# Kernel optimization log

Hardware: AMD Instinct MI355X
Metric: run time of the kernel (lower is better)

The kernel has to match this reference:

```python
import jax, jax.numpy as jnp
import numpy as np

B, S, E = 8, 2048, 768
N, H = 12, 64
INIT = 0.02
IGNORE = -100000.0


def setup_inputs() -> dict:
    key = jax.random.key(0)
    ks = jax.random.split(key, 5)
    return {
        "normalized_resid_pre": jax.random.normal(ks[0], (B, S, E), jnp.float32),
        "W_Q": jax.random.normal(ks[1], (N, E, H), jnp.float32) * INIT,
        "W_K": jax.random.normal(ks[2], (N, E, H), jnp.float32) * INIT,
        "W_V": jax.random.normal(ks[3], (N, E, H), jnp.float32) * INIT,
        "W_O": jax.random.normal(ks[4], (N, H, E), jnp.float32) * INIT,
        "b_Q": jnp.zeros((N, H), jnp.float32),
        "b_K": jnp.zeros((N, H), jnp.float32),
        "b_V": jnp.zeros((N, H), jnp.float32),
        "b_O": jnp.zeros((E,), jnp.float32),
    }


def reference(normalized_resid_pre, W_Q, W_K, W_V, W_O, b_Q, b_K, b_V, b_O):
    x = normalized_resid_pre
    b, s, e = x.shape
    d_head = W_Q.shape[-1]
    q = jnp.einsum('bse,neh->bsnh', x, W_Q) + b_Q  # [b, sq, n, h]
    k = jnp.einsum('bse,neh->bsnh', x, W_K) + b_K
    v = jnp.einsum('bse,neh->bsnh', x, W_V) + b_V
    scores = jnp.einsum('bqnh,bknh->bnqk', q, k) / jnp.sqrt(jnp.float32(d_head))
    mask = jnp.tril(jnp.ones((s, s), jnp.float32))  # [sq, sk]
    masked = mask * scores + (1.0 - mask) * IGNORE
    probs = jax.nn.softmax(masked, axis=-1)
    z = jnp.einsum('bnqk,bknh->bqnh', probs, v)
    # sum over heads of per-head output projection + bias
    out = jnp.einsum('bqnh,nhe->bqe', z, W_O) + b_O
    return out
```

## Files before the change

kernel.cpp:

```cpp
#include <hip/hip_runtime.h>
#include <hip/hip_bf16.h>
#include <stdint.h>


#define B_ 8
#define S_ 2048
#define E_ 768
#define NHEADS 12
#define HD 64
#define BS (B_*S_)
#define NHD (NHEADS*HD)

typedef short bf16x8 __attribute__((ext_vector_type(8)));
typedef short bf16x4 __attribute__((ext_vector_type(4)));
typedef float f32x4  __attribute__((ext_vector_type(4)));
typedef __hip_bfloat16 bf16;

typedef const __attribute__((address_space(1))) char* as1_t;
typedef __attribute__((address_space(3))) char* as3_t;

__device__ __forceinline__ f32x4 mfma16(bf16x8 a, bf16x8 b, f32x4 c) {
    return __builtin_amdgcn_mfma_f32_16x16x32_bf16(a, b, c, 0, 0, 0);
}
__device__ __forceinline__ bf16x8 ld8(const bf16* p) {
    return *reinterpret_cast<const bf16x8*>(p);
}
__device__ __forceinline__ void gload16(const bf16* g, bf16* l) {
    __builtin_amdgcn_global_load_lds((as1_t)g, (as3_t)l, 16, 0, 0);
}
__device__ __forceinline__ bf16x8 pack8(f32x4 a, f32x4 b) {
    union { bf16x8 v; __hip_bfloat162 h[4]; } u;
    u.h[0] = __float22bfloat162_rn(make_float2(a[0], a[1]));
    u.h[1] = __float22bfloat162_rn(make_float2(a[2], a[3]));
    u.h[2] = __float22bfloat162_rn(make_float2(b[0], b[1]));
    u.h[3] = __float22bfloat162_rn(make_float2(b[2], b[3]));
    return u.v;
}

__global__ __launch_bounds__(256) void prep_kernel(
    const float* __restrict__ x,  const float* __restrict__ Wq,
    const float* __restrict__ Wk, const float* __restrict__ Wv,
    const float* __restrict__ Wo,
    bf16* __restrict__ xb,  bf16* __restrict__ WqT, bf16* __restrict__ WkT,
    bf16* __restrict__ WvT, bf16* __restrict__ WoT)
{
    const int tid = blockIdx.x * 256 + threadIdx.x;
    const int nth = gridDim.x * 256;
    for (int i = tid; i < BS*E_; i += nth)
        xb[i] = __float2bfloat16(x[i]);
    for (int i = tid; i < NHD*E_; i += nth) {
        const int c = i / E_;
        const int e = i - c*E_;
        const int n = c >> 6, h = c & 63;
        const int src = (n*E_ + e)*HD + h;
        WqT[i] = __float2bfloat16(Wq[src]);
        WkT[i] = __float2bfloat16(Wk[src]);
        WvT[i] = __float2bfloat16(Wv[src]);
        WoT[e*NHD + c] = __float2bfloat16(Wo[i]);
    }
}


#define FENCE() asm volatile("" ::: "memory")
#define LGKM0() do { asm volatile("s_waitcnt lgkmcnt(0)" ::: "memory"); \
                     __builtin_amdgcn_sched_barrier(0); } while (0)
#define VMCNT0() asm volatile("s_waitcnt vmcnt(0)" ::: "memory")
#define MIN11(x) ((x) < 11 ? (x) : 11)

#define A_ELEM(kh, rg) (((kh)*8 + (rg))*512)
#define B_ELEM(kh, rg) (((kh)*12 + (rg))*512)

#define STG_A(dst, gbase, kt) do {                                                \
    const bf16* _s = (gbase) + (size_t)(w*16 + l16)*768 + (kt)*64 + quad*8;       \
    gload16(_s,      &(dst)[A_ELEM(0, w)]);                                       \
    gload16(_s + 32, &(dst)[A_ELEM(1, w)]);                                       \
} while (0)

#define STG_B(dst, gbase, kt) do {                                                \
    const bf16* _s = (gbase) + (size_t)(l16)*768 + (kt)*64 + quad*8;              \
    const int _k1 = (w < 4) ? 0 : 1;                                              \
    const int _r1 = (w < 4) ? (w + 8) : (w - 4);                                  \
    gload16(_s + (size_t)(w*16)*768,        &(dst)[B_ELEM(0, w)]);                \
    gload16(_s + (size_t)(_r1*16)*768 + _k1*32, &(dst)[B_ELEM(_k1, _r1)]);        \
    gload16(_s + (size_t)((w+4)*16)*768 + 32,   &(dst)[B_ELEM(1, w+4)]);          \
} while (0)

#define KTILE(bufA, bufB, nA, nB, ktn, Ab, Bb) do {                               \
                                          \
    _Pragma("unroll") for (int n = 0; n < 3; ++n)                                 \
    _Pragma("unroll") for (int ks = 0; ks < 2; ++ks)                              \
        bfr[n][ks] = ld8(&(bufB)[((ks)*12 + wn*3 + n)*512 + lane*8]);             \
    {                                                                             \
        bf16x8 afr[2][2];                                                         \
        _Pragma("unroll") for (int m = 0; m < 2; ++m)                             \
        _Pragma("unroll") for (int ks = 0; ks < 2; ++ks)                          \
            afr[m][ks] = ld8(&(bufA)[((ks)*8 + wm*4 + m)*512 + lane*8]);          \
        STG_A(nA, Ab, ktn);                                                       \
        LGKM0();                                                                  \
        __builtin_amdgcn_s_setprio(1);                                            \
        _Pragma("unroll") for (int m = 0; m < 2; ++m)                             \
        _Pragma("unroll") for (int n = 0; n < 3; ++n)                             \
        _Pragma("unroll") for (int ks = 0; ks < 2; ++ks)                          \
            acc[m][n] = mfma16(afr[m][ks], bfr[n][ks], acc[m][n]);                \
        __builtin_amdgcn_s_setprio(0);                                            \
    }                                                                             \
                                                    \
    {                                                                             \
        bf16x8 afr[2][2];                                                         \
        _Pragma("unroll") for (int m = 0; m < 2; ++m)                             \
        _Pragma("unroll") for (int ks = 0; ks < 2; ++ks)                          \
            afr[m][ks] = ld8(&(bufA)[((ks)*8 + wm*4 + 2 + m)*512 + lane*8]);      \
        STG_B(nB, Bb, ktn);                                                       \
        LGKM0();                                                                  \
        __builtin_amdgcn_s_setprio(1);                                            \
        _Pragma("unroll") for (int m = 0; m < 2; ++m)                             \
        _Pragma("unroll") for (int n = 0; n < 3; ++n)                             \
        _Pragma("unroll") for (int ks = 0; ks < 2; ++ks)                          \
            acc[2+m][n] = mfma16(afr[m][ks], bfr[n][ks], acc[2+m][n]);            \
        __builtin_amdgcn_s_setprio(0);                                            \
    }                                                                             \
    VMCNT0();                                                                     \
    FENCE(); __builtin_amdgcn_s_barrier(); FENCE();                               \
} while (0)

#define GEMM128_BODY(Ab, Bb)                                                      \
    f32x4 acc[4][3];                                                              \
    _Pragma("unroll") for (int mf = 0; mf < 4; ++mf)                              \
    _Pragma("unroll") for (int nf = 0; nf < 3; ++nf)                              \
        acc[mf][nf] = (f32x4){0.f, 0.f, 0.f, 0.f};                                \
    bf16x8 bfr[3][2];                                                             \
    STG_A(sA0, Ab, 0); STG_B(sB0, Bb, 0);                                         \
    VMCNT0();                                                                     \
    FENCE(); __builtin_amdgcn_s_barrier(); FENCE();                               \
    _Pragma("unroll 1")                                                           \
    for (int i2 = 0; i2 < 6; ++i2) {                                              \
        const int kt0 = 2*i2;                                                     \
        KTILE(sA0, sB0, sA1, sB1, kt0 + 1,        Ab, Bb);                        \
        KTILE(sA1, sB1, sA0, sB0, MIN11(kt0 + 2), Ab, Bb);                        \
    }

__global__ __launch_bounds__(512, 4) void qkv_gemm256(
    const bf16* __restrict__ xb, const bf16* __restrict__ WT,
    const float* __restrict__ bq, const float* __restrict__ bk, const float* __restrict__ bv,
    bf16* __restrict__ Qb, bf16* __restrict__ Kb, bf16* __restrict__ VTb)
{
    __shared__ __align__(16) bf16 sA0[8192];
    __shared__ __align__(16) bf16 sA1[8192];
    __shared__ __align__(16) bf16 sB0[12288];
    __shared__ __align__(16) bf16 sB1[12288];

    const int tm = blockIdx.x, tn = blockIdx.y;
    const int lane = threadIdx.x & 63;
    const int w    = threadIdx.x >> 6;
    const int wm = w >> 2, wn = w & 3;
    const int l16 = lane & 15, quad = lane >> 4;
    const bf16* Ab = xb + (size_t)tm*128*E_;
    const bf16* Bb = WT + (size_t)tn*192*E_;

    GEMM128_BODY(Ab, Bb);

    const int mat = tn >> 2;
    const int cloc0 = (tn & 3)*192 + wn*48;
    const float* bias = (mat==0) ? bq : (mat==1) ? bk : bv;
    const float scale = (mat==0) ? 0.125f * 1.44269504088896340736f : 1.0f;
    bf16* dstQK = (mat==0) ? Qb : Kb;
    #pragma unroll
    for (int nf = 0; nf < 3; ++nf) {
        const int col = cloc0 + nf*16 + l16;
        const int hn = col >> 6, h = col & 63;
        const float bb = bias[col];
        #pragma unroll
        for (int mf = 0; mf < 4; ++mf) {
            const int row = tm*128 + wm*64 + mf*16 + quad*4;
            const int bi = row >> 11;
            const int s  = row & (S_-1);
            if (mat < 2) {
                bf16* d = dstQK + ((size_t)(bi*NHEADS + hn)*S_ + s)*HD + h;
                #pragma unroll
                for (int r = 0; r < 4; ++r)
                    d[(size_t)r*HD] = __float2bfloat16((acc[mf][nf][r] + bb)*scale);
            } else {
                bf16* d = VTb + ((size_t)(bi*NHEADS + hn)*HD + h)*S_ + s;
                union { bf16x4 v; bf16 e[4]; } u;
                #pragma unroll
                for (int r = 0; r < 4; ++r) u.e[r] = __float2bfloat16(acc[mf][nf][r] + bb);
                *reinterpret_cast<bf16x4*>(d) = u.v;
            }
        }
    }
}

__global__ __launch_bounds__(512, 4) void out_gemm256(
    const bf16* __restrict__ Z, const bf16* __restrict__ WoT,
    const float* __restrict__ bo, float* __restrict__ out)
{
    __shared__ __align__(16) bf16 sA0[8192];
    __shared__ __align__(16) bf16 sA1[8192];
    __shared__ __align__(16) bf16 sB0[12288];
    __shared__ __align__(16) bf16 sB1[12288];

    const int tm = blockIdx.x, tn = blockIdx.y;
    const int lane = threadIdx.x & 63;
    const int w    = threadIdx.x >> 6;
    const int wm = w >> 2, wn = w & 3;
    const int l16 = lane & 15, quad = lane >> 4;
    const bf16* Ab = Z   + (size_t)tm*128*NHD;
    const bf16* Bb = WoT + (size_t)tn*192*NHD;

    GEMM128_BODY(Ab, Bb);

    #pragma unroll
    for (int nf = 0; nf < 3; ++nf) {
        const int col = tn*192 + wn*48 + nf*16 + l16;
        const float bb = bo[col];
        #pragma unroll
        for (int mf = 0; mf < 4; ++mf) {
            const int row = tm*128 + wm*64 + mf*16 + quad*4;
            float* d = out + (size_t)row*E_ + col;
            #pragma unroll
            for (int r = 0; r < 4; ++r)
                d[(size_t)r*E_] = acc[mf][nf][r] + bb;
        }
    }
}

__global__ __launch_bounds__(256, 3) void attn_kernel(
    const bf16* __restrict__ Qb, const bf16* __restrict__ Kb,
    const bf16* __restrict__ VTb, bf16* __restrict__ Z)
{
    __shared__ __align__(16) bf16 sK[2][64*64];
    __shared__ __align__(16) bf16 sV[2][64*64];

    const int id = blockIdx.x;
    const int bx = id / 96;
    const int g  = id - bx*96;
    const int hn = g % NHEADS, b = g / NHEADS;
    const int tid  = threadIdx.x;
    const int w    = tid >> 6;
    const int lane = tid & 63;
    const int l16 = lane & 15, quad = lane >> 4;
    const size_t bn = (size_t)b*NHEADS + hn;

    const bf16* Qbase = Qb  + bn*S_*HD;
    const bf16* Kbase = Kb  + bn*S_*HD;
    const bf16* Vbase = VTb + bn*HD*S_;

    const int mA = tid, mB = tid + 256;
    const int rA = mA >> 3, cgA = mA & 7;
    const int rB = mB >> 3, cgB = mB & 7;
    const int slA = (rA*8 + ((cgA + rA + (rA>>3)) & 7)) * 8;
    const int slB = (rB*8 + ((cgB + rB + (rB>>3)) & 7)) * 8;
    const size_t vofA = (size_t)rA*S_ + cgA*8;
    const size_t vofB = (size_t)rB*S_ + cgB*8;

    const int kperm = (l16 >> 2)*8 + (l16 & 3);
    int kidx[2][2][2];
    #pragma unroll
    for (int c=0;c<2;c++)
        #pragma unroll
        for (int bg=0;bg<2;bg++)
            #pragma unroll
            for (int hf=0;hf<2;hf++) {
                const int r = 32*c + 4*bg + kperm;
                const int q = hf*4 + quad;
                kidx[c][bg][hf] = (r*8 + ((q + r + (r>>3)) & 7)) * 8;
            }
    int vidx[4][2];
    #pragma unroll
    for (int ht=0;ht<4;ht++)
        #pragma unroll
        for (int c=0;c<2;c++) {
            const int rho = ht*16 + l16;
            const int q = c*4 + quad;
            vidx[ht][c] = (rho*8 + ((q + rho + (rho>>3)) & 7)) * 8;
        }

    #pragma unroll
    for (int half = 0; half < 2; ++half) {
        const int qblk = half ? (S_/128 - 1 - bx) : bx;
        const int ktb  = 2*qblk + 1;
        const int ktw  = 2*qblk + (w >> 1);
        const int qbase = qblk*128 + w*32;

        bf16x8 bqf[2][2];
        #pragma unroll
        for (int qi=0;qi<2;qi++)
            #pragma unroll
            for (int hf=0;hf<2;hf++)
                bqf[qi][hf] = ld8(Qbase + (size_t)(qbase + qi*16 + l16)*HD + hf*32 + quad*8);

        f32x4 acc[2][4];
        #pragma unroll
        for (int qi=0;qi<2;qi++)
            #pragma unroll
            for (int ht=0;ht<4;ht++) acc[qi][ht] = (f32x4){0.f,0.f,0.f,0.f};
        float lsum[2] = {0.f, 0.f};

        bf16x8 k0 = ld8(Kbase + (size_t)mA*8);
        bf16x8 k1 = ld8(Kbase + (size_t)mB*8);
        bf16x8 v0 = ld8(Vbase + vofA);
        bf16x8 v1 = ld8(Vbase + vofB);
        *reinterpret_cast<bf16x8*>(&sK[0][slA]) = k0;
        *reinterpret_cast<bf16x8*>(&sK[0][slB]) = k1;
        *reinterpret_cast<bf16x8*>(&sV[0][slA]) = v0;
        *reinterpret_cast<bf16x8*>(&sV[0][slB]) = v1;
        __syncthreads();

        for (int kt = 0; kt <= ktb; ++kt) {
            if (kt < ktb) {
                const size_t kt1 = (size_t)(kt+1)*64;
                k0 = ld8(Kbase + kt1*HD + (size_t)mA*8);
                k1 = ld8(Kbase + kt1*HD + (size_t)mB*8);
                v0 = ld8(Vbase + vofA + kt1);
                v1 = ld8(Vbase + vofB + kt1);
            }
            if (kt <= ktw) {
                const bf16* kb = sK[kt & 1];
                const bf16* vb = sV[kt & 1];
                #pragma unroll
                for (int c=0;c<2;c++) {
                    const bf16x8 akA0 = ld8(kb + kidx[c][0][0]);
                    const bf16x8 akA1 = ld8(kb + kidx[c][0][1]);
                    const bf16x8 akB0 = ld8(kb + kidx[c][1][0]);
                    const bf16x8 akB1 = ld8(kb + kidx[c][1][1]);
                    bf16x8 av[4];
                    #pragma unroll
                    for (int ht=0;ht<4;ht++) av[ht] = ld8(vb + vidx[ht][c]);

                    #pragma unroll
                    for (int qi=0;qi<2;qi++) {
                        f32x4 s0 = (f32x4){0.f,0.f,0.f,0.f};
                        s0 = mfma16(akA0, bqf[qi][0], s0);
                        s0 = mfma16(akA1, bqf[qi][1], s0);
                        f32x4 s1 = (f32x4){0.f,0.f,0.f,0.f};
                        s1 = mfma16(akB0, bqf[qi][0], s1);
                        s1 = mfma16(akB1, bqf[qi][1], s1);
                        if (kt == ktw) {
                            const int q  = qbase + qi*16 + l16;
                            const int kb0 = kt*64 + c*32 + quad*8;
                            #pragma unroll
                            for (int r=0;r<4;r++) {
                                s0[r] = (kb0 + r     > q) ? -1e30f : s0[r];
                                s1[r] = (kb0 + 4 + r > q) ? -1e30f : s1[r];
                            }
                        }
                        float ls = 0.f;
                        #pragma unroll
                        for (int r=0;r<4;r++) {
                            s0[r] = __builtin_amdgcn_exp2f(s0[r]);
                            s1[r] = __builtin_amdgcn_exp2f(s1[r]);
                            ls += s0[r] + s1[r];
                        }
                        lsum[qi] += ls;
                        const bf16x8 pf = pack8(s0, s1);
                        #pragma unroll
                        for (int ht=0;ht<4;ht++)
                            acc[qi][ht] = mfma16(av[ht], pf, acc[qi][ht]);
                    }
                }
            }
            if (kt < ktb) {
                const int nb = (kt+1) & 1;
                *reinterpret_cast<bf16x8*>(&sK[nb][slA]) = k0;
                *reinterpret_cast<bf16x8*>(&sK[nb][slB]) = k1;
                *reinterpret_cast<bf16x8*>(&sV[nb][slA]) = v0;
                *reinterpret_cast<bf16x8*>(&sV[nb][slB]) = v1;
            }
            __syncthreads();
        }

        #pragma unroll
        for (int qi=0;qi<2;qi++) {
            float rs = lsum[qi];
            rs += __shfl_xor(rs, 16, 64);
            rs += __shfl_xor(rs, 32, 64);
            const float inv_l = 1.0f / rs;
            const int q = qbase + qi*16 + l16;
            bf16* zp = Z + ((size_t)b*S_ + q)*NHD + (size_t)hn*HD + quad*4;
            #pragma unroll
            for (int ht=0;ht<4;ht++) {
                union { bf16x4 v; bf16 e[4]; } u;
                #pragma unroll
                for (int r=0;r<4;r++) u.e[r] = __float2bfloat16(acc[qi][ht][r] * inv_l);
                *reinterpret_cast<bf16x4*>(zp + ht*16) = u.v;
            }
        }
    }
}

extern "C" void kernel_launch(void* const* d_in, const int* in_sizes, int n_in,
                              void* d_out, int out_size, void* d_ws, size_t ws_size,
                              hipStream_t stream)
{
    const float* x  = (const float*)d_in[0];
    const float* Wq = (const float*)d_in[1];
    const float* Wk = (const float*)d_in[2];
    const float* Wv = (const float*)d_in[3];
    const float* Wo = (const float*)d_in[4];
    const float* bq = (const float*)d_in[5];
    const float* bk = (const float*)d_in[6];
    const float* bv = (const float*)d_in[7];
    const float* bo = (const float*)d_in[8];
    float* out = (float*)d_out;

    char* ws = (char*)d_ws;
    size_t off = 0;
    auto alloc = [&](size_t bytes){ char* p = ws + off; off += (bytes + 255) & ~(size_t)255; return p; };
    bf16* xb  = (bf16*)alloc((size_t)BS*E_*2);
    bf16* WT  = (bf16*)alloc((size_t)3*NHD*E_*2);
    bf16* WoT = (bf16*)alloc((size_t)E_*NHD*2);
    bf16* Qb  = (bf16*)alloc((size_t)BS*NHD*2);
    bf16* Kb  = (bf16*)alloc((size_t)BS*NHD*2);
    bf16* VTb = (bf16*)alloc((size_t)BS*NHD*2);
    bf16* Zb  = (bf16*)alloc((size_t)BS*NHD*2);

    bf16* WqT = WT;
    bf16* WkT = WT + (size_t)NHD*E_;
    bf16* WvT = WT + (size_t)2*NHD*E_;

    prep_kernel<<<4096, 256, 0, stream>>>(x, Wq, Wk, Wv, Wo, xb, WqT, WkT, WvT, WoT);
    qkv_gemm256<<<dim3(BS/128, 12), 512, 0, stream>>>(xb, WT, bq, bk, bv, Qb, Kb, VTb);
    attn_kernel<<<768, 256, 0, stream>>>(Qb, Kb, VTb, Zb);
    out_gemm256<<<dim3(BS/128, E_/192), 512, 0, stream>>>(Zb, WoT, bo, out);
}
```

Measured before the change: 242.5 us.

## Replace LDS-staged GEMMs with direct global-to-register MFMA loads

Both projection GEMMs drop the double-buffered global_load_lds staging through shared memory. Each wave now loads its A and B fragments straight from global memory into registers for every k-tile. Tiles shrink to 128x96 with 4 waves per block, which doubles the grid. This removes LDS traffic and barriers, but each wave reloads operands with no sharing through shared memory, so it depends on cache hits and adds global-memory latency.

```diff
diff --git a/kernel.cpp b/kernel.cpp
--- a/kernel.cpp
+++ b/kernel.cpp
@@ -16,17 +16,11 @@
 typedef float f32x4  __attribute__((ext_vector_type(4)));
 typedef __hip_bfloat16 bf16;
 
-typedef const __attribute__((address_space(1))) char* as1_t;
-typedef __attribute__((address_space(3))) char* as3_t;
-
 __device__ __forceinline__ f32x4 mfma16(bf16x8 a, bf16x8 b, f32x4 c) {
     return __builtin_amdgcn_mfma_f32_16x16x32_bf16(a, b, c, 0, 0, 0);
 }
 __device__ __forceinline__ bf16x8 ld8(const bf16* p) {
     return *reinterpret_cast<const bf16x8*>(p);
-}
-__device__ __forceinline__ void gload16(const bf16* g, bf16* l) {
-    __builtin_amdgcn_global_load_lds((as1_t)g, (as3_t)l, 16, 0, 0);
 }
 __device__ __forceinline__ bf16x8 pack8(f32x4 a, f32x4 b) {
     union { bf16x8 v; __hip_bfloat162 h[4]; } u;
@@ -61,106 +55,43 @@
 }
 
 
-#define FENCE() asm volatile("" ::: "memory")
-#define LGKM0() do { asm volatile("s_waitcnt lgkmcnt(0)" ::: "memory"); \
-                     __builtin_amdgcn_sched_barrier(0); } while (0)
-#define VMCNT0() asm volatile("s_waitcnt vmcnt(0)" ::: "memory")
-#define MIN11(x) ((x) < 11 ? (x) : 11)
-
-#define A_ELEM(kh, rg) (((kh)*8 + (rg))*512)
-#define B_ELEM(kh, rg) (((kh)*12 + (rg))*512)
-
-#define STG_A(dst, gbase, kt) do {                                                \
-    const bf16* _s = (gbase) + (size_t)(w*16 + l16)*768 + (kt)*64 + quad*8;       \
-    gload16(_s,      &(dst)[A_ELEM(0, w)]);                                       \
-    gload16(_s + 32, &(dst)[A_ELEM(1, w)]);                                       \
-} while (0)
-
-#define STG_B(dst, gbase, kt) do {                                                \
-    const bf16* _s = (gbase) + (size_t)(l16)*768 + (kt)*64 + quad*8;              \
-    const int _k1 = (w < 4) ? 0 : 1;                                              \
-    const int _r1 = (w < 4) ? (w + 8) : (w - 4);                                  \
-    gload16(_s + (size_t)(w*16)*768,        &(dst)[B_ELEM(0, w)]);                \
-    gload16(_s + (size_t)(_r1*16)*768 + _k1*32, &(dst)[B_ELEM(_k1, _r1)]);        \
-    gload16(_s + (size_t)((w+4)*16)*768 + 32,   &(dst)[B_ELEM(1, w+4)]);          \
-} while (0)
-
-#define KTILE(bufA, bufB, nA, nB, ktn, Ab, Bb) do {                               \
-                                          \
-    _Pragma("unroll") for (int n = 0; n < 3; ++n)                                 \
-    _Pragma("unroll") for (int ks = 0; ks < 2; ++ks)                              \
-        bfr[n][ks] = ld8(&(bufB)[((ks)*12 + wn*3 + n)*512 + lane*8]);             \
-    {                                                                             \
-        bf16x8 afr[2][2];                                                         \
-        _Pragma("unroll") for (int m = 0; m < 2; ++m)                             \
-        _Pragma("unroll") for (int ks = 0; ks < 2; ++ks)                          \
-            afr[m][ks] = ld8(&(bufA)[((ks)*8 + wm*4 + m)*512 + lane*8]);          \
-        STG_A(nA, Ab, ktn);                                                       \
-        LGKM0();                                                                  \
-        __builtin_amdgcn_s_setprio(1);                                            \
-        _Pragma("unroll") for (int m = 0; m < 2; ++m)                             \
-        _Pragma("unroll") for (int n = 0; n < 3; ++n)                             \
-        _Pragma("unroll") for (int ks = 0; ks < 2; ++ks)                          \
-            acc[m][n] = mfma16(afr[m][ks], bfr[n][ks], acc[m][n]);                \
-        __builtin_amdgcn_s_setprio(0);                                            \
-    }                                                                             \
-                                                    \
-    {                                                                             \
-        bf16x8 afr[2][2];                                                         \
-        _Pragma("unroll") for (int m = 0; m < 2; ++m)                             \
-        _Pragma("unroll") for (int ks = 0; ks < 2; ++ks)                          \
-            afr[m][ks] = ld8(&(bufA)[((ks)*8 + wm*4 + 2 + m)*512 + lane*8]);      \
-        STG_B(nB, Bb, ktn);                                                       \
-        LGKM0();                                                                  \
-        __builtin_amdgcn_s_setprio(1);                                            \
-        _Pragma("unroll") for (int m = 0; m < 2; ++m)                             \
-        _Pragma("unroll") for (int n = 0; n < 3; ++n)                             \
-        _Pragma("unroll") for (int ks = 0; ks < 2; ++ks)                          \
-            acc[2+m][n] = mfma16(afr[m][ks], bfr[n][ks], acc[2+m][n]);            \
-        __builtin_amdgcn_s_setprio(0);                                            \
-    }                                                                             \
-    VMCNT0();                                                                     \
-    FENCE(); __builtin_amdgcn_s_barrier(); FENCE();                               \
-} while (0)
-
-#define GEMM128_BODY(Ab, Bb)                                                      \
+#define DIRECT_GEMM_BODY(Ath, Bth)                                                \
     f32x4 acc[4][3];                                                              \
     _Pragma("unroll") for (int mf = 0; mf < 4; ++mf)                              \
     _Pragma("unroll") for (int nf = 0; nf < 3; ++nf)                              \
         acc[mf][nf] = (f32x4){0.f, 0.f, 0.f, 0.f};                                \
-    bf16x8 bfr[3][2];                                                             \
-    STG_A(sA0, Ab, 0); STG_B(sB0, Bb, 0);                                         \
-    VMCNT0();                                                                     \
-    FENCE(); __builtin_amdgcn_s_barrier(); FENCE();                               \
-    _Pragma("unroll 1")                                                           \
-    for (int i2 = 0; i2 < 6; ++i2) {                                              \
-        const int kt0 = 2*i2;                                                     \
-        KTILE(sA0, sB0, sA1, sB1, kt0 + 1,        Ab, Bb);                        \
-        KTILE(sA1, sB1, sA0, sB0, MIN11(kt0 + 2), Ab, Bb);                        \
-    }
-
-__global__ __launch_bounds__(512, 4) void qkv_gemm256(
+    _Pragma("unroll")                                                             \
+    for (int kt = 0; kt < 12; ++kt) {                                             \
+        bf16x8 af[4][2], bf[3][2];                                                \
+        _Pragma("unroll") for (int m = 0; m < 4; ++m)                             \
+        _Pragma("unroll") for (int ks = 0; ks < 2; ++ks)                          \
+            af[m][ks] = ld8((Ath) + (size_t)(m*16)*768 + kt*64 + ks*32);          \
+        _Pragma("unroll") for (int n = 0; n < 3; ++n)                             \
+        _Pragma("unroll") for (int ks = 0; ks < 2; ++ks)                          \
+            bf[n][ks] = ld8((Bth) + (size_t)(n*16)*768 + kt*64 + ks*32);          \
+        _Pragma("unroll") for (int ks = 0; ks < 2; ++ks)                          \
+        _Pragma("unroll") for (int m = 0; m < 4; ++m)                             \
+        _Pragma("unroll") for (int n = 0; n < 3; ++n)                             \
+            acc[m][n] = mfma16(af[m][ks], bf[n][ks], acc[m][n]);                  \
+    }
+
+__global__ __launch_bounds__(256, 3) void qkv_gemm_d(
     const bf16* __restrict__ xb, const bf16* __restrict__ WT,
     const float* __restrict__ bq, const float* __restrict__ bk, const float* __restrict__ bv,
     bf16* __restrict__ Qb, bf16* __restrict__ Kb, bf16* __restrict__ VTb)
 {
-    __shared__ __align__(16) bf16 sA0[8192];
-    __shared__ __align__(16) bf16 sA1[8192];
-    __shared__ __align__(16) bf16 sB0[12288];
-    __shared__ __align__(16) bf16 sB1[12288];
-
     const int tm = blockIdx.x, tn = blockIdx.y;
     const int lane = threadIdx.x & 63;
     const int w    = threadIdx.x >> 6;
-    const int wm = w >> 2, wn = w & 3;
+    const int wm = w >> 1, wn = w & 1;
     const int l16 = lane & 15, quad = lane >> 4;
-    const bf16* Ab = xb + (size_t)tm*128*E_;
-    const bf16* Bb = WT + (size_t)tn*192*E_;
-
-    GEMM128_BODY(Ab, Bb);
-
-    const int mat = tn >> 2;
-    const int cloc0 = (tn & 3)*192 + wn*48;
+    const bf16* Ath = xb + (size_t)(tm*128 + wm*64 + l16)*768 + quad*8;
+    const bf16* Bth = WT + (size_t)(tn*96  + wn*48 + l16)*768 + quad*8;
+
+    DIRECT_GEMM_BODY(Ath, Bth);
+
+    const int mat = tn >> 3;
+    const int cloc0 = (tn & 7)*96 + wn*48;
     const float* bias = (mat==0) ? bq : (mat==1) ? bk : bv;
     const float scale = (mat==0) ? 0.125f * 1.44269504088896340736f : 1.0f;
     bf16* dstQK = (mat==0) ? Qb : Kb;
@@ -190,28 +121,23 @@
     }
 }
 
-__global__ __launch_bounds__(512, 4) void out_gemm256(
+__global__ __launch_bounds__(256, 3) void out_gemm_d(
     const bf16* __restrict__ Z, const bf16* __restrict__ WoT,
     const float* __restrict__ bo, float* __restrict__ out)
 {
-    __shared__ __align__(16) bf16 sA0[8192];
-    __shared__ __align__(16) bf16 sA1[8192];
-    __shared__ __align__(16) bf16 sB0[12288];
-    __shared__ __align__(16) bf16 sB1[12288];
-
     const int tm = blockIdx.x, tn = blockIdx.y;
     const int lane = threadIdx.x & 63;
     const int w    = threadIdx.x >> 6;
-    const int wm = w >> 2, wn = w & 3;
+    const int wm = w >> 1, wn = w & 1;
     const int l16 = lane & 15, quad = lane >> 4;
-    const bf16* Ab = Z   + (size_t)tm*128*NHD;
-    const bf16* Bb = WoT + (size_t)tn*192*NHD;
-
-    GEMM128_BODY(Ab, Bb);
+    const bf16* Ath = Z   + (size_t)(tm*128 + wm*64 + l16)*768 + quad*8;
+    const bf16* Bth = WoT + (size_t)(tn*96  + wn*48 + l16)*768 + quad*8;
+
+    DIRECT_GEMM_BODY(Ath, Bth);
 
     #pragma unroll
     for (int nf = 0; nf < 3; ++nf) {
-        const int col = tn*192 + wn*48 + nf*16 + l16;
+        const int col = tn*96 + wn*48 + nf*16 + l16;
         const float bb = bo[col];
         #pragma unroll
         for (int mf = 0; mf < 4; ++mf) {
@@ -419,7 +345,7 @@
     bf16* WvT = WT + (size_t)2*NHD*E_;
 
     prep_kernel<<<4096, 256, 0, stream>>>(x, Wq, Wk, Wv, Wo, xb, WqT, WkT, WvT, WoT);
-    qkv_gemm256<<<dim3(BS/128, 12), 512, 0, stream>>>(xb, WT, bq, bk, bv, Qb, Kb, VTb);
+    qkv_gemm_d<<<dim3(BS/128, 24), 256, 0, stream>>>(xb, WT, bq, bk, bv, Qb, Kb, VTb);
     attn_kernel<<<768, 256, 0, stream>>>(Qb, Kb, VTb, Zb);
-    out_gemm256<<<dim3(BS/128, E_/192), 512, 0, stream>>>(Zb, WoT, bo, out);
-}
+    out_gemm_d<<<dim3(BS/128, 8), 256, 0, stream>>>(Zb, WoT, bo, out);
+}
```

Result: slower. 413.2 us (+70.4%).
